# Kernel tuning notes

Measured on AMD Instinct MI355X. Metric: run time of the kernel, lower is better.

The kernel has to match this reference:

```python
import jax, jax.numpy as jnp
import numpy as np

N_OBJ = 256   # number of RoIs/objects
C = 151       # num_obj_classes (Visual Genome)
H = 512       # hidden_dim == output_dim
T = 3         # time_step


def setup_inputs() -> dict:
    key = jax.random.key(0)
    ks = jax.random.split(key, 12)
    s = jnp.float32(0.02)

    def lin(k, out_dim, in_dim):
        k1, k2 = jax.random.split(k)
        w = jax.random.normal(k1, (out_dim, in_dim), jnp.float32) * s
        b = jax.random.normal(k2, (out_dim,), jnp.float32) * s
        return w, b

    inp = {}
    inp['input_ggnn'] = jax.random.normal(ks[0], (N_OBJ, H), jnp.float32)
    inp['matrix'] = jax.random.uniform(ks[1], (C, C), jnp.float32)
    for i, name in enumerate(['eq3_w', 'eq3_u', 'eq4_w', 'eq4_u', 'eq5_w', 'eq5_u']):
        in_dim = 2 * H if name.endswith('_w') else H
        w, b = lin(ks[2 + i], H, in_dim)
        inp['w_' + name] = w
        inp['b_' + name] = b
    w, b = lin(ks[8], H, 2 * H)
    inp['w_out'], inp['b_out'] = w, b
    w, b = lin(ks[9], C, C * H)
    inp['w_cls'], inp['b_cls'] = w, b
    return inp


def _ggnn_obj(input_ggnn, matrix,
              w_eq3_w, b_eq3_w, w_eq3_u, b_eq3_u,
              w_eq4_w, b_eq4_w, w_eq4_u, b_eq4_u,
              w_eq5_w, b_eq5_w, w_eq5_u, b_eq5_u,
              w_out, b_out, w_cls, b_cls):
    n = input_ggnn.shape[0]
    # hidden[i, c] = input_ggnn[i] for every class slot c  -> [N, C, H]
    hidden0 = jnp.broadcast_to(input_ggnn[:, None, :], (n, C, H))

    def step(hidden, _):
        hidden_sum = hidden.sum(axis=0)                # [C, H]
        x = hidden_sum[None, :, :] - hidden            # [N, C, H]
        # matrix.T @ x_i  and  matrix @ x_i, vectorized over N
        av1 = jnp.einsum('cd,nch->ndh', matrix, x)     # M^T propagation
        av2 = jnp.einsum('dc,nch->ndh', matrix, x)     # M propagation
        av = jnp.concatenate([av1, av2], axis=-1).reshape(n * C, 2 * H)
        h = hidden.reshape(n * C, H)
        zv = jax.nn.sigmoid(av @ w_eq3_w.T + b_eq3_w + h @ w_eq3_u.T + b_eq3_u)
        rv = jax.nn.sigmoid(av @ w_eq4_w.T + b_eq4_w + h @ w_eq4_u.T + b_eq4_u)
        hv = jnp.tanh(av @ w_eq5_w.T + b_eq5_w + (rv * h) @ w_eq5_u.T + b_eq5_u)
        h = (1.0 - zv) * h + zv * hv
        return h.reshape(n, C, H), None

    hidden, _ = jax.lax.scan(step, hidden0, None, length=T)

    inp_rep = hidden0.reshape(n * C, H)                # input repeated per class slot
    out = jnp.concatenate([hidden.reshape(n * C, H), inp_rep], axis=1)  # [N*C, 2H]
    out = jax.nn.relu(out @ w_out.T + b_out)           # [N*C, H]
    obj_dists = out.reshape(n, C * H) @ w_cls.T + b_cls  # [N, C]
    return obj_dists


def reference(input_ggnn, matrix,
              w_eq3_w, b_eq3_w, w_eq3_u, b_eq3_u,
              w_eq4_w, b_eq4_w, w_eq4_u, b_eq4_u,
              w_eq5_w, b_eq5_w, w_eq5_u, b_eq5_u,
              w_out, b_out, w_cls, b_cls):
    return _ggnn_obj(input_ggnn, matrix,
                     w_eq3_w, b_eq3_w, w_eq3_u, b_eq3_u,
                     w_eq4_w, b_eq4_w, w_eq4_u, b_eq4_u,
                     w_eq5_w, b_eq5_w, w_eq5_u, b_eq5_u,
                     w_out, b_out, w_cls, b_cls)
```

## Files before the change

kernel.cpp:

```cpp
#include <hip/hip_runtime.h>


#define C_     151
#define H_     512
#define NOBJ   256
#define NR     38656
#define NCH    64
#define CH     9664
#define CHP    9728
#define KPAD   160
#define KLDS   168
#define KA     2560
#define KV     3584
#define KB     2560

typedef _Float16 half8 __attribute__((ext_vector_type(8)));
typedef _Float16 half4 __attribute__((ext_vector_type(4)));
typedef float    f32x4 __attribute__((ext_vector_type(4)));

__device__ __forceinline__ float sigm(float x) { return 1.f / (1.f + expf(-x)); }

__device__ __forceinline__ void gload16(const void* g, void* l) {
    __builtin_amdgcn_global_load_lds(
        (const __attribute__((address_space(1))) void*)g,
        (__attribute__((address_space(3))) void*)l, 16, 0, 0);
}

__device__ __forceinline__ int kqswz(int s) {
    return 8 * (((s & 3) + 8 - ((s >> 2) & 3) - ((s >> 4) & 3)) & 3);
}
__device__ __forceinline__ int fraswz(int lane) {
    const int lb = lane & 15;
    return lb * 32 + 8 * (((lane >> 4) + lb + (lb >> 2)) & 3);
}

__device__ __forceinline__ half8 loadA8(const _Float16* p) { return *(const half8*)p; }
__device__ __forceinline__ half8 loadA8(const float* p) {
    f32x4 a = *(const f32x4*)p;
    f32x4 b = *(const f32x4*)(p + 4);
    half8 o;
    #pragma unroll
    for (int j = 0; j < 4; ++j) { o[j] = (_Float16)a[j]; o[4 + j] = (_Float16)b[j]; }
    return o;
}

template<int OP, typename AT, bool DUPK>
__global__ __launch_bounds__(256, 2)
void gemm_kernel(const AT* __restrict__ A, int lda,
                 const _Float16* __restrict__ B, int ldb,
                 void* __restrict__ Out, int ldo,
                 const float* __restrict__ bias,
                 const float* __restrict__ bias2,
                 int kchunk, int chunkStride)
{
    constexpr bool A16 = (sizeof(AT) == 2);
    __shared__ _Float16 sA[128 * 32];
    __shared__ _Float16 sB[128 * 32];
    const int tid  = threadIdx.x;
    const int lane = tid & 63;
    const int w    = tid >> 6;
    const int m0   = blockIdx.x * 128;
    const int n0   = blockIdx.y * 128;
    const int kbase = blockIdx.z * kchunk;

    const int s0 = tid, s1 = tid + 256;
    const AT* Ap0 = A + (size_t)(m0 + (s0 >> 2)) * lda + kqswz(s0);
    const AT* Ap1 = A + (size_t)(m0 + (s1 >> 2)) * lda + kqswz(s1);
    const _Float16* Bp0 = B + (size_t)(n0 + (s0 >> 2)) * ldb + kbase + kqswz(s0);
    const _Float16* Bp1 = B + (size_t)(n0 + (s1 >> 2)) * ldb + kbase + kqswz(s1);
    const int la0 = 8 * s0;
    const int la1 = 8 * s1;
    _Float16* lA0 = &sA[w * 512];
    _Float16* lA1 = &sA[2048 + w * 512];
    _Float16* lB0 = &sB[w * 512];
    _Float16* lB1 = &sB[2048 + w * 512];

    f32x4 acc[4][4];
    #pragma unroll
    for (int i = 0; i < 4; ++i)
        #pragma unroll
        for (int j = 0; j < 4; ++j)
            #pragma unroll
            for (int r = 0; r < 4; ++r) acc[i][j][r] = 0.f;

    const int mrow = (w >> 1) * 64;
    const int ncol = (w & 1) * 64;
    const int fra  = fraswz(lane);

    for (int k0 = 0; k0 < kchunk; k0 += 32) {
        int kA;
        if (DUPK) kA = (k0 < 2048) ? k0 : ((k0 < 3072) ? k0 - 2048 : k0 - 1024);
        else      kA = kbase + k0;
        if constexpr (A16) {
            __syncthreads();
            gload16(Ap0 + kA, lA0);
            gload16(Ap1 + kA, lA1);
            gload16(Bp0 + k0, lB0);
            gload16(Bp1 + k0, lB1);
            __syncthreads();
        } else {
            half8 va0 = loadA8(Ap0 + kA);
            half8 va1 = loadA8(Ap1 + kA);
            half8 vb0 = *(const half8*)(Bp0 + k0);
            half8 vb1 = *(const half8*)(Bp1 + k0);
            __syncthreads();
            *(half8*)&sA[la0] = va0;
            *(half8*)&sA[la1] = va1;
            *(half8*)&sB[la0] = vb0;
            *(half8*)&sB[la1] = vb1;
            __syncthreads();
        }
        half8 af[4], bf[4];
        #pragma unroll
        for (int i = 0; i < 4; ++i)
            af[i] = *(const half8*)&sA[(mrow + i * 16) * 32 + fra];
        #pragma unroll
        for (int i = 0; i < 4; ++i)
            bf[i] = *(const half8*)&sB[(ncol + i * 16) * 32 + fra];
        #pragma unroll
        for (int mi = 0; mi < 4; ++mi)
            #pragma unroll
            for (int ni = 0; ni < 4; ++ni)
                acc[mi][ni] = __builtin_amdgcn_mfma_f32_16x16x32_f16(af[mi], bf[ni], acc[mi][ni], 0, 0, 0);
    }

    const size_t zoff = (size_t)blockIdx.z * (size_t)chunkStride;
    #pragma unroll
    for (int mi = 0; mi < 4; ++mi) {
        #pragma unroll
        for (int ni = 0; ni < 4; ++ni) {
            #pragma unroll
            for (int r = 0; r < 4; ++r) {
                const int row = m0 + mrow + mi * 16 + (lane >> 4) * 4 + r;
                const int col = n0 + ncol + ni * 16 + (lane & 15);
                float v = acc[mi][ni][r];
                const size_t o = zoff + (size_t)row * ldo + col;
                if (OP == 0) {
                    ((float*)Out)[o] = v;
                } else if (OP == 1) {
                    ((_Float16*)Out)[o] = (_Float16)v;
                } else {
                    const unsigned n = (unsigned)row / 151u;
                    v += bias[col] + bias2[n * 512u + col];
                    v = v > 0.f ? v : 0.f;
                    ((_Float16*)Out)[o] = (_Float16)v;
                }
            }
        }
    }
}

__global__ __launch_bounds__(512, 2)
void gemm256(const _Float16* __restrict__ A, const _Float16* __restrict__ B,
             _Float16* __restrict__ Out)
{
    constexpr int LDA = KA;
    constexpr int LDB = KB;
    constexpr int LDO = 1536;
    constexpr int NT  = KV / 64;
    __shared__ _Float16 lds[2][32768];

    const int tid  = threadIdx.x;
    const int lane = tid & 63;
    const int w    = tid >> 6;

    const int lin  = blockIdx.y * gridDim.x + blockIdx.x;
    const int xcd  = lin & 7;
    const int sub  = lin >> 3;
    const int wgid = (xcd < 4 ? xcd * 29 : 4 * 29 + (xcd - 4) * 28) + sub;
    const int m0   = (wgid / 6) * 256;
    const int n0   = (wgid % 6) * 256;

    const int tr  = tid >> 3;
    const int swz = ((tid & 7) ^ (tr & 7)) << 3;
    const _Float16* Ap = A + (size_t)(m0 + tr) * LDA + swz;
    const _Float16* Bp = B + (size_t)(n0 + tr) * LDB + swz;
    const int ldsbase = w << 9;

    auto stA = [&](int buf, int kAb, int r0) {
        gload16(Ap + (size_t)r0 * LDA + kAb, &lds[buf][r0 * 64 + ldsbase]);
    };
    auto stB = [&](int buf, int kBb, int r0) {
        gload16(Bp + (size_t)r0 * LDB + kBb, &lds[buf][16384 + r0 * 64 + ldsbase]);
    };

    const int lb = lane & 15;
    const int lq = lane >> 4;
    auto frag = [&](const _Float16* base, int row0, int ks) -> half8 {
        const int row = row0 + lb;
        const int kg  = ks * 4 + lq;
        return *(const half8*)&base[row * 64 + ((kg ^ (row & 7)) << 3)];
    };

    const int wm = (w >> 2) * 128;
    const int wn = (w & 3) * 64;

    f32x4 acc[8][4];
    #pragma unroll
    for (int i = 0; i < 8; ++i)
        #pragma unroll
        for (int j = 0; j < 4; ++j)
            #pragma unroll
            for (int r = 0; r < 4; ++r) acc[i][j][r] = 0.f;

    half8 a[4][2], bA[2][2], bB[2][2];

#define PHASE_MFMA(AF, BF, MO, NO) do {                                         \
    __builtin_amdgcn_s_setprio(1);                                              \
    _Pragma("unroll")                                                           \
    for (int i = 0; i < 4; ++i) {                                               \
        _Pragma("unroll")                                                       \
        for (int j = 0; j < 2; ++j) {                                           \
            _Pragma("unroll")                                                   \
            for (int ks = 0; ks < 2; ++ks)                                      \
                acc[(MO) + i][(NO) + j] =                                       \
                    __builtin_amdgcn_mfma_f32_16x16x32_f16(                     \
                        AF[i][ks], BF[j][ks], acc[(MO) + i][(NO) + j], 0, 0, 0);\
        }                                                                       \
    }                                                                           \
    __builtin_amdgcn_s_setprio(0);                                              \
} while (0)

    stB(0, 0, 0);  stB(0, 0, 64);  stB(0, 0, 128); stB(0, 0, 192);
    stA(0, 0, 0);  stA(0, 0, 64);  stA(0, 0, 128); stA(0, 0, 192);

    for (int t = 0; t < NT; ++t) {
        const _Float16* sA = &lds[t & 1][0];
        const _Float16* sB = &lds[t & 1][16384];

        asm volatile("s_waitcnt vmcnt(0)" ::: "memory");
        __builtin_amdgcn_s_barrier();
        __builtin_amdgcn_sched_barrier(0);

        if (t + 1 < NT) {
            const int kk  = (t + 1) * 64;
            const int kAb = (kk < 2048) ? kk : ((kk < 3072) ? kk - 2048 : kk - 1024);
            const int kBb = (kk < 1024) ? kk : kk - 1024;
            const int nb  = (t + 1) & 1;
            stB(nb, kBb, 0); stB(nb, kBb, 64); stB(nb, kBb, 128); stB(nb, kBb, 192);
            stA(nb, kAb, 0); stA(nb, kAb, 64); stA(nb, kAb, 128); stA(nb, kAb, 192);
        }

        #pragma unroll
        for (int i = 0; i < 4; ++i) {
            a[i][0] = frag(sA, wm + i * 16, 0);
            a[i][1] = frag(sA, wm + i * 16, 1);
        }
        #pragma unroll
        for (int j = 0; j < 2; ++j) {
            bA[j][0] = frag(sB, wn + j * 16, 0);
            bA[j][1] = frag(sB, wn + j * 16, 1);
            bB[j][0] = frag(sB, wn + 32 + j * 16, 0);
            bB[j][1] = frag(sB, wn + 32 + j * 16, 1);
        }
        PHASE_MFMA(a, bA, 0, 0);
        PHASE_MFMA(a, bB, 0, 2);

        #pragma unroll
        for (int i = 0; i < 4; ++i) {
            a[i][0] = frag(sA, wm + 64 + i * 16, 0);
            a[i][1] = frag(sA, wm + 64 + i * 16, 1);
        }
        PHASE_MFMA(a, bA, 4, 0);
        PHASE_MFMA(a, bB, 4, 2);
    }
#undef PHASE_MFMA

    #pragma unroll
    for (int mi = 0; mi < 8; ++mi) {
        #pragma unroll
        for (int ni = 0; ni < 4; ++ni) {
            #pragma unroll
            for (int r = 0; r < 4; ++r) {
                const int row = m0 + wm + mi * 16 + (lane >> 4) * 4 + r;
                const int col = n0 + wn + ni * 16 + (lane & 15);
                Out[(size_t)row * LDO + col] = (_Float16)acc[mi][ni][r];
            }
        }
    }
}

__global__ __launch_bounds__(256, 2)
void mix_kernel(const float* __restrict__ hid, const float* __restrict__ S,
                const _Float16* __restrict__ MTh, const _Float16* __restrict__ MTl,
                const _Float16* __restrict__ Mrh, const _Float16* __restrict__ Mrl,
                _Float16* __restrict__ AVH, int cbase)
{
    __shared__ _Float16 sxh[64 * KLDS];
    __shared__ _Float16 sxl[64 * KLDS];
    const int n  = blockIdx.x;
    const int h0 = blockIdx.y * 64;
    const int tid = threadIdx.x;

    #pragma unroll
    for (int i = 0; i < 5; ++i) {
        const int s  = tid + 256 * i;
        const int c  = s >> 3;
        const int hg = s & 7;
        half8 oh, ol;
        if (c < C_) {
            const float* hp = &hid[(size_t)(cbase + n * C_ + c) * H_ + h0 + hg * 8];
            const float* sp = &S[c * H_ + h0 + hg * 8];
            half8 hh;
            #pragma unroll
            for (int j = 0; j < 8; ++j) {
                const float hv = hp[j];
                const float x = sp[j] - hv;
                const _Float16 hi = (_Float16)x;
                oh[j] = hi;
                ol[j] = (_Float16)(x - (float)hi);
                hh[j] = (_Float16)hv;
            }
            *(half8*)&AVH[(size_t)(n * C_ + c) * KA + 2048 + h0 + hg * 8] = hh;
        } else {
            #pragma unroll
            for (int j = 0; j < 8; ++j) { oh[j] = (_Float16)0.f; ol[j] = (_Float16)0.f; }
        }
        #pragma unroll
        for (int j = 0; j < 8; ++j) {
            sxh[(hg * 8 + j) * KLDS + c] = oh[j];
            sxl[(hg * 8 + j) * KLDS + c] = ol[j];
        }
    }
    __syncthreads();

    const int lane = tid & 63;
    const int w    = tid >> 6;
    const _Float16* Mhi = (w >> 1) ? Mrh : MTh;
    const _Float16* Mlo = (w >> 1) ? Mrl : MTl;
    const int hb = (w & 1) * 32;

    f32x4 acc[10][2];
    #pragma unroll
    for (int i = 0; i < 10; ++i)
        #pragma unroll
        for (int j = 0; j < 2; ++j)
            #pragma unroll
            for (int r = 0; r < 4; ++r) acc[i][j][r] = 0.f;

    #pragma unroll
    for (int pass = 0; pass < 3; ++pass) {
        const _Float16* Ma = (pass == 2) ? Mlo : Mhi;
        const _Float16* X  = (pass == 1) ? sxl : sxh;
        #pragma unroll
        for (int kk = 0; kk < 5; ++kk) {
            const int k0 = kk * 32;
            half8 bf[2];
            #pragma unroll
            for (int ht = 0; ht < 2; ++ht)
                bf[ht] = *(const half8*)&X[(hb + ht * 16 + (lane & 15)) * KLDS + k0 + 8 * (lane >> 4)];
            #pragma unroll
            for (int dt = 0; dt < 10; ++dt) {
                half8 af = *(const half8*)&Ma[(dt * 16 + (lane & 15)) * KPAD + k0 + 8 * (lane >> 4)];
                acc[dt][0] = __builtin_amdgcn_mfma_f32_16x16x32_f16(af, bf[0], acc[dt][0], 0, 0, 0);
                acc[dt][1] = __builtin_amdgcn_mfma_f32_16x16x32_f16(af, bf[1], acc[dt][1], 0, 0, 0);
            }
        }
    }

    const int mixoff = (w >> 1) * 512;
    #pragma unroll
    for (int dt = 0; dt < 10; ++dt) {
        #pragma unroll
        for (int ht = 0; ht < 2; ++ht) {
            #pragma unroll
            for (int r = 0; r < 4; ++r) {
                const int d = dt * 16 + (lane >> 4) * 4 + r;
                if (d < C_) {
                    const int h = h0 + hb + ht * 16 + (lane & 15);
                    const float v = acc[dt][ht][r];
                    const _Float16 hi = (_Float16)v;
                    const _Float16 lo = (_Float16)(v - (float)hi);
                    _Float16* rowp = AVH + (size_t)(n * C_ + d) * KA + mixoff + h;
                    rowp[0]    = hi;
                    rowp[1024] = lo;
                }
            }
        }
    }
}


__global__ void k_sreduce(const float* __restrict__ hid, float* __restrict__ Stmp)
{
    const int c  = blockIdx.x;
    const int g  = blockIdx.y;
    const int hw = threadIdx.x;
    const float* p = hid + (size_t)c * H_ + hw * 8;
    float s[8];
    #pragma unroll
    for (int j = 0; j < 8; ++j) s[j] = 0.f;
    const size_t stride = (size_t)C_ * H_;
    for (int n = g * 32; n < g * 32 + 32; ++n) {
        f32x4 a = *(const f32x4*)(p + (size_t)n * stride);
        f32x4 b = *(const f32x4*)(p + (size_t)n * stride + 4);
        #pragma unroll
        for (int j = 0; j < 4; ++j) { s[j] += a[j]; s[4 + j] += b[j]; }
    }
    float* o = Stmp + (size_t)g * (C_ * H_) + c * H_ + hw * 8;
    *(f32x4*)o       = f32x4{s[0], s[1], s[2], s[3]};
    *(f32x4*)(o + 4) = f32x4{s[4], s[5], s[6], s[7]};
}

__global__ void k_sfold(const float* __restrict__ Stmp, float* __restrict__ S)
{
    const int idx = blockIdx.x * 256 + threadIdx.x;
    float s = 0.f;
    #pragma unroll
    for (int g = 0; g < 8; ++g) s += Stmp[(size_t)g * (C_ * H_) + idx];
    S[idx] = s;
}

__global__ void k_ew1(_Float16* __restrict__ pre, const float* __restrict__ hid,
                      const float* __restrict__ bz, const float* __restrict__ br, int cbase)
{
    const int idx = blockIdx.x * 256 + threadIdx.x;
    const unsigned r = idx >> 7;
    const int o4 = (idx & 127) << 2;
    const size_t base = (size_t)r * 1536;
    half4 zp = *(const half4*)&pre[base + o4];
    half4 rp = *(const half4*)&pre[base + 512 + o4];
    f32x4 hd = *(const f32x4*)&hid[(size_t)(cbase + r) * H_ + o4];
    f32x4 bz4 = *(const f32x4*)&bz[o4];
    f32x4 br4 = *(const f32x4*)&br[o4];
    half4 zs, rh;
    #pragma unroll
    for (int j = 0; j < 4; ++j) {
        float z = sigm((float)zp[j] + bz4[j]);
        float rr = sigm((float)rp[j] + br4[j]);
        zs[j] = (_Float16)z;
        rh[j] = (_Float16)(rr * hd[j]);
    }
    *(half4*)&pre[base + o4] = zs;
    *(half4*)&pre[base + 512 + o4] = rh;
}

__global__ void k_ew2(const _Float16* __restrict__ pre, const _Float16* __restrict__ p5a,
                      const _Float16* __restrict__ p5b,
                      float* __restrict__ hid, const float* __restrict__ b5, int cbase)
{
    const int idx = blockIdx.x * 256 + threadIdx.x;
    const unsigned r = idx >> 7;
    const int o4 = (idx & 127) << 2;
    const size_t base = (size_t)r * 1536;
    half4 w5 = *(const half4*)&pre[base + 1024 + o4];
    half4 pa = *(const half4*)&p5a[(size_t)r * H_ + o4];
    half4 pb = *(const half4*)&p5b[(size_t)r * H_ + o4];
    half4 zz = *(const half4*)&pre[base + o4];
    f32x4 hd = *(const f32x4*)&hid[(size_t)(cbase + r) * H_ + o4];
    f32x4 b54 = *(const f32x4*)&b5[o4];
    #pragma unroll
    for (int j = 0; j < 4; ++j) {
        float t = tanhf((float)w5[j] + (float)pa[j] + (float)pb[j] + b54[j]);
        float z = (float)zz[j];
        hd[j] = (1.f - z) * hd[j] + z * t;
    }
    *(f32x4*)&hid[(size_t)(cbase + r) * H_ + o4] = hd;
}


__global__ void prep_wbig(const float* w3w, const float* w3u,
                          const float* w4w, const float* w4u,
                          const float* w5w, const float* w5u,
                          _Float16* __restrict__ Wbig)
{
    const int idx = blockIdx.x * 256 + threadIdx.x;
    const int op = idx / KB;
    const int j = idx - op * KB;
    const int g = op >> 9, o = op & 511;
    const float* ww = (g == 0) ? w3w : (g == 1) ? w4w : w5w;
    const float* wu = (g == 0) ? w3u : (g == 1) ? w4u : w5u;
    _Float16 out;
    if (j < 1024) {
        out = (_Float16)ww[o * 1024 + j];
    } else if (j < 2048) {
        const float v = ww[o * 1024 + (j - 1024)];
        const _Float16 hi = (_Float16)v;
        out = (_Float16)(v - (float)hi);
    } else {
        out = (g < 2) ? (_Float16)wu[o * 512 + (j - 2048)] : (_Float16)0.f;
    }
    Wbig[idx] = out;
}

__global__ void prep_m(const float* __restrict__ matrix,
                       _Float16* __restrict__ MTh, _Float16* __restrict__ MTl,
                       _Float16* __restrict__ Mrh, _Float16* __restrict__ Mrl)
{
    const int idx = blockIdx.x * 256 + threadIdx.x;
    const int d = idx / KPAD, c = idx - d * KPAD;
    float vT = 0.f, vR = 0.f;
    if (d < C_ && c < C_) { vT = matrix[c * C_ + d]; vR = matrix[d * C_ + c]; }
    const _Float16 th = (_Float16)vT;
    const _Float16 rh = (_Float16)vR;
    MTh[idx] = th; MTl[idx] = (_Float16)(vT - (float)th);
    Mrh[idx] = rh; Mrl[idx] = (_Float16)(vR - (float)rh);
}

__global__ void prep_wout(const float* __restrict__ wout,
                          _Float16* __restrict__ WL, _Float16* __restrict__ WR)
{
    const int idx = blockIdx.x * 256 + threadIdx.x;
    const int o = idx >> 9, j = idx & 511;
    WL[idx] = (_Float16)wout[o * 1024 + j];
    WR[idx] = (_Float16)wout[o * 1024 + 512 + j];
}

__global__ void prep_wcls(const float* __restrict__ wcls, _Float16* __restrict__ w16)
{
    const int k = blockIdx.x * 256 + threadIdx.x;
    const int d = blockIdx.y;
    w16[(size_t)d * (C_ * H_) + k] = (_Float16)wcls[(size_t)d * (C_ * H_) + k];
}

__global__ void k_cast(const float* __restrict__ src, _Float16* __restrict__ dst, int n)
{
    const int i = blockIdx.x * 256 + threadIdx.x;
    if (i < n) dst[i] = (_Float16)src[i];
}

__global__ void prep_bias(const float* b3w, const float* b3u, const float* b4w,
                          const float* b4u, const float* b5w, const float* b5u,
                          float* bz, float* br, float* b5)
{
    const int i = threadIdx.x;
    bz[i] = b3w[i] + b3u[i];
    br[i] = b4w[i] + b4u[i];
    b5[i] = b5w[i] + b5u[i];
}

__global__ void prep_hid(const float* __restrict__ input, float* __restrict__ hid)
{
    const int idx = blockIdx.x * 256 + threadIdx.x;
    const unsigned row = idx >> 7;
    const int h4 = (idx & 127) << 2;
    const unsigned n = row / 151u;
    f32x4 v = *(const f32x4*)&input[(size_t)n * H_ + h4];
    *(f32x4*)&hid[(size_t)row * H_ + h4] = v;
}

__global__ void k_reduce(const float* __restrict__ partial, const float* __restrict__ bcls,
                         float* __restrict__ out)
{
    const int idx = blockIdx.x * 256 + threadIdx.x;
    const unsigned n = (unsigned)idx / 151u;
    const unsigned d = (unsigned)idx - n * 151u;
    float s = 0.f;
    for (int z = 0; z < C_; ++z)
        s += partial[(size_t)z * (NOBJ * 256) + n * 256 + d];
    out[idx] = s + bcls[d];
}


extern "C" void kernel_launch(void* const* d_in, const int* in_sizes, int n_in,
                              void* d_out, int out_size, void* d_ws, size_t ws_size,
                              hipStream_t stream)
{
    const float* input  = (const float*)d_in[0];
    const float* matrix = (const float*)d_in[1];
    const float* w3w = (const float*)d_in[2];
    const float* b3w = (const float*)d_in[3];
    const float* w3u = (const float*)d_in[4];
    const float* b3u = (const float*)d_in[5];
    const float* w4w = (const float*)d_in[6];
    const float* b4w = (const float*)d_in[7];
    const float* w4u = (const float*)d_in[8];
    const float* b4u = (const float*)d_in[9];
    const float* w5w = (const float*)d_in[10];
    const float* b5w = (const float*)d_in[11];
    const float* w5u = (const float*)d_in[12];
    const float* b5u = (const float*)d_in[13];
    const float* wout = (const float*)d_in[14];
    const float* bout = (const float*)d_in[15];
    const float* wcls = (const float*)d_in[16];
    const float* bcls = (const float*)d_in[17];
    float* obj = (float*)d_out;

    char* ws = (char*)d_ws;
    size_t off = 0;
    auto take = [&](size_t bytes) -> char* {
        off = (off + 255) & ~(size_t)255;
        char* p = ws + off;
        off += bytes;
        return p;
    };

    _Float16* Wbig  = (_Float16*)take((size_t)1536 * KB * 2);
    _Float16* MTh   = (_Float16*)take((size_t)KPAD * KPAD * 2);
    _Float16* MTl   = (_Float16*)take((size_t)KPAD * KPAD * 2);
    _Float16* Mrh   = (_Float16*)take((size_t)KPAD * KPAD * 2);
    _Float16* Mrl   = (_Float16*)take((size_t)KPAD * KPAD * 2);
    _Float16* W5u16 = (_Float16*)take((size_t)512 * 512 * 2);
    _Float16* WL16  = (_Float16*)take((size_t)512 * 512 * 2);
    _Float16* WR16  = (_Float16*)take((size_t)512 * 512 * 2);
    _Float16* in16  = (_Float16*)take((size_t)256 * 512 * 2);
    float*    bz    = (float*)take(512 * 4);
    float*    br    = (float*)take(512 * 4);
    float*    b5    = (float*)take(512 * 4);
    float*    Stmp  = (float*)take((size_t)8 * C_ * H_ * 4);
    float*    S32   = (float*)take((size_t)C_ * H_ * 4);
    float*    base  = (float*)take((size_t)256 * 512 * 4);
    float*    hid32 = (float*)take((size_t)NR * H_ * 4);
    _Float16* AVH   = (_Float16*)take((size_t)CHP * KA * 2);
    _Float16* prec  = (_Float16*)take((size_t)CHP * 1536 * 2);
    _Float16* p5u = AVH;
    _Float16* OUT16 = AVH;
    _Float16* Wcls16 = (_Float16*)hid32;
    float* partial = (float*)((char*)hid32 + (size_t)NOBJ * C_ * H_ * 2);

    (void)in_sizes; (void)n_in; (void)out_size; (void)ws_size;

    prep_wbig<<<dim3((1536 * KB) / 256), 256, 0, stream>>>(w3w, w3u, w4w, w4u, w5w, w5u, Wbig);
    prep_m<<<dim3((KPAD * KPAD) / 256), 256, 0, stream>>>(matrix, MTh, MTl, Mrh, Mrl);
    k_cast<<<dim3((512 * 512) / 256), 256, 0, stream>>>(w5u, W5u16, 512 * 512);
    prep_wout<<<dim3((512 * 512) / 256), 256, 0, stream>>>(wout, WL16, WR16);
    k_cast<<<dim3((256 * 512) / 256), 256, 0, stream>>>(input, in16, 256 * 512);
    prep_bias<<<dim3(1), 512, 0, stream>>>(b3w, b3u, b4w, b4u, b5w, b5u, bz, br, b5);
    prep_hid<<<dim3((NR * 128) / 256), 256, 0, stream>>>(input, hid32);
    gemm_kernel<0, _Float16, false><<<dim3(2, 4, 1), 256, 0, stream>>>(
        in16, 512, WR16, 512, base, 512, nullptr, nullptr, 512, 0);

    for (int t = 0; t < 3; ++t) {
        k_sreduce<<<dim3(C_, 8), 64, 0, stream>>>(hid32, Stmp);
        k_sfold<<<dim3((C_ * H_) / 256), 256, 0, stream>>>(Stmp, S32);
        for (int cc = 0; cc < 4; ++cc) {
            const int cbase = cc * CH;
            mix_kernel<<<dim3(NCH, 8), 256, 0, stream>>>(
                hid32, S32, MTh, MTl, Mrh, Mrl, AVH, cbase);
            gemm256<<<dim3(CHP / 256, 1536 / 256, 1), 512, 0, stream>>>(
                AVH, Wbig, prec);
            k_ew1<<<dim3((CH * 128) / 256), 256, 0, stream>>>(prec, hid32, bz, br, cbase);
            gemm_kernel<1, _Float16, false><<<dim3(CHP / 128, 4, 2), 256, 0, stream>>>(
                prec + 512, 1536, W5u16, 512, p5u, 512, nullptr, nullptr, 256, CHP * 512);
            k_ew2<<<dim3((CH * 128) / 256), 256, 0, stream>>>(
                prec, p5u, p5u + (size_t)CHP * 512, hid32, b5, cbase);
        }
    }

    gemm_kernel<2, float, false><<<dim3(NR / 128, 512 / 128, 1), 256, 0, stream>>>(
        hid32, 512, WL16, 512, OUT16, 512, bout, base, 512, 0);

    prep_wcls<<<dim3((C_ * H_) / 256, C_), 256, 0, stream>>>(wcls, Wcls16);
    gemm_kernel<0, _Float16, false><<<dim3(NOBJ / 128, 256 / 128, C_), 256, 0, stream>>>(
        OUT16, C_ * H_, Wcls16, C_ * H_, partial, 256, nullptr, nullptr, 512, NOBJ * 256);
    k_reduce<<<dim3(NR / 256), 256, 0, stream>>>(partial, bcls, obj);
}
```

Measured before the change: 2.420 ms.

## Restructure gemm256 into 4-stage LDS pipeline with K=32 tiles and register prefetch

The gemm256 main loop changes from a double-buffered K=64 tile with a full vmcnt(0) wait each iteration to a 4-buffer ring of K=32 tiles. Global-to-LDS loads run three tiles ahead, and fragments for the next tile are read into alternate register sets while the current MFMAs run. The aim is to hide global load latency and LDS read latency behind MFMA work. In exchange there are twice as many barriers per K, more registers for the doubled fragment sets, and a redundant dummy stage load at the tail.

```diff
diff --git a/kernel.cpp b/kernel.cpp
--- a/kernel.cpp
+++ b/kernel.cpp
@@ -157,8 +157,8 @@
     constexpr int LDA = KA;
     constexpr int LDB = KB;
     constexpr int LDO = 1536;
-    constexpr int NT  = KV / 64;
-    __shared__ _Float16 lds[2][32768];
+    constexpr int NT  = KV / 32;
+    __shared__ _Float16 lds[4 * 16384];
 
     const int tid  = threadIdx.x;
     const int lane = tid & 63;
@@ -171,25 +171,25 @@
     const int m0   = (wgid / 6) * 256;
     const int n0   = (wgid % 6) * 256;
 
-    const int tr  = tid >> 3;
-    const int swz = ((tid & 7) ^ (tr & 7)) << 3;
+    const int tr  = tid >> 2;
+    const int swz = (((tid & 3) ^ (tr & 3)) << 3);
     const _Float16* Ap = A + (size_t)(m0 + tr) * LDA + swz;
     const _Float16* Bp = B + (size_t)(n0 + tr) * LDB + swz;
-    const int ldsbase = w << 9;
-
-    auto stA = [&](int buf, int kAb, int r0) {
-        gload16(Ap + (size_t)r0 * LDA + kAb, &lds[buf][r0 * 64 + ldsbase]);
-    };
-    auto stB = [&](int buf, int kBb, int r0) {
-        gload16(Bp + (size_t)r0 * LDB + kBb, &lds[buf][16384 + r0 * 64 + ldsbase]);
+    const int ldsw = w << 9;
+
+    auto stage = [&](int buf, int kAb, int kBb) {
+        _Float16* L = &lds[buf * 16384];
+        gload16(Ap + kAb,                     L + ldsw);
+        gload16(Ap + (size_t)128 * LDA + kAb, L + 4096 + ldsw);
+        gload16(Bp + kBb,                     L + 8192 + ldsw);
+        gload16(Bp + (size_t)128 * LDB + kBb, L + 12288 + ldsw);
     };
 
     const int lb = lane & 15;
     const int lq = lane >> 4;
-    auto frag = [&](const _Float16* base, int row0, int ks) -> half8 {
+    auto frag = [&](const _Float16* base, int row0) -> half8 {
         const int row = row0 + lb;
-        const int kg  = ks * 4 + lq;
-        return *(const half8*)&base[row * 64 + ((kg ^ (row & 7)) << 3)];
+        return *(const half8*)&base[row * 32 + ((lq ^ (row & 3)) << 3)];
     };
 
     const int wm = (w >> 2) * 128;
@@ -203,68 +203,64 @@
             #pragma unroll
             for (int r = 0; r < 4; ++r) acc[i][j][r] = 0.f;
 
-    half8 a[4][2], bA[2][2], bB[2][2];
-
-#define PHASE_MFMA(AF, BF, MO, NO) do {                                         \
+    half8 aE[8], bE[4], aO[8], bO[4];
+
+    auto kAmap = [](int kk) { return (kk < 2048) ? kk : ((kk < 3072) ? kk - 2048 : kk - 1024); };
+    auto kBmap = [](int kk) { return (kk < 1024) ? kk : kk - 1024; };
+
+#define READF(T1, AN, BN) do {                                                  \
+    const _Float16* bufA_ = &lds[((T1) & 3) * 16384];                           \
+    const _Float16* bufB_ = bufA_ + 8192;                                       \
+    _Pragma("unroll")                                                           \
+    for (int i = 0; i < 8; ++i) AN[i] = frag(bufA_, wm + i * 16);               \
+    _Pragma("unroll")                                                           \
+    for (int j = 0; j < 4; ++j) BN[j] = frag(bufB_, wn + j * 16);               \
+} while (0)
+
+#define MFMA32(AC, BC) do {                                                     \
     __builtin_amdgcn_s_setprio(1);                                              \
     _Pragma("unroll")                                                           \
-    for (int i = 0; i < 4; ++i) {                                               \
+    for (int i = 0; i < 8; ++i)                                                 \
         _Pragma("unroll")                                                       \
-        for (int j = 0; j < 2; ++j) {                                           \
-            _Pragma("unroll")                                                   \
-            for (int ks = 0; ks < 2; ++ks)                                      \
-                acc[(MO) + i][(NO) + j] =                                       \
-                    __builtin_amdgcn_mfma_f32_16x16x32_f16(                     \
-                        AF[i][ks], BF[j][ks], acc[(MO) + i][(NO) + j], 0, 0, 0);\
-        }                                                                       \
-    }                                                                           \
+        for (int j = 0; j < 4; ++j)                                             \
+            acc[i][j] = __builtin_amdgcn_mfma_f32_16x16x32_f16(                 \
+                AC[i], BC[j], acc[i][j], 0, 0, 0);                              \
     __builtin_amdgcn_s_setprio(0);                                              \
 } while (0)
 
-    stB(0, 0, 0);  stB(0, 0, 64);  stB(0, 0, 128); stB(0, 0, 192);
-    stA(0, 0, 0);  stA(0, 0, 64);  stA(0, 0, 128); stA(0, 0, 192);
-
-    for (int t = 0; t < NT; ++t) {
-        const _Float16* sA = &lds[t & 1][0];
-        const _Float16* sB = &lds[t & 1][16384];
-
-        asm volatile("s_waitcnt vmcnt(0)" ::: "memory");
-        __builtin_amdgcn_s_barrier();
-        __builtin_amdgcn_sched_barrier(0);
-
-        if (t + 1 < NT) {
-            const int kk  = (t + 1) * 64;
-            const int kAb = (kk < 2048) ? kk : ((kk < 3072) ? kk - 2048 : kk - 1024);
-            const int kBb = (kk < 1024) ? kk : kk - 1024;
-            const int nb  = (t + 1) & 1;
-            stB(nb, kBb, 0); stB(nb, kBb, 64); stB(nb, kBb, 128); stB(nb, kBb, 192);
-            stA(nb, kAb, 0); stA(nb, kAb, 64); stA(nb, kAb, 128); stA(nb, kAb, 192);
-        }
-
-        #pragma unroll
-        for (int i = 0; i < 4; ++i) {
-            a[i][0] = frag(sA, wm + i * 16, 0);
-            a[i][1] = frag(sA, wm + i * 16, 1);
-        }
-        #pragma unroll
-        for (int j = 0; j < 2; ++j) {
-            bA[j][0] = frag(sB, wn + j * 16, 0);
-            bA[j][1] = frag(sB, wn + j * 16, 1);
-            bB[j][0] = frag(sB, wn + 32 + j * 16, 0);
-            bB[j][1] = frag(sB, wn + 32 + j * 16, 1);
-        }
-        PHASE_MFMA(a, bA, 0, 0);
-        PHASE_MFMA(a, bB, 0, 2);
-
-        #pragma unroll
-        for (int i = 0; i < 4; ++i) {
-            a[i][0] = frag(sA, wm + 64 + i * 16, 0);
-            a[i][1] = frag(sA, wm + 64 + i * 16, 1);
-        }
-        PHASE_MFMA(a, bA, 4, 0);
-        PHASE_MFMA(a, bB, 4, 2);
-    }
-#undef PHASE_MFMA
+#define TILE_STEP(T, AC, BC, AN, BN) do {                                       \
+    asm volatile("s_waitcnt vmcnt(4)" ::: "memory");                            \
+    __builtin_amdgcn_s_barrier();                                               \
+    __builtin_amdgcn_sched_barrier(0);                                          \
+    { int kks = ((T) + 3) * 32;                                                 \
+      if (kks >= KV) kks = 0;              \
+      stage(((T) + 3) & 3, kAmap(kks), kBmap(kks)); }                           \
+    READF((T) + 1, AN, BN);                                                     \
+    asm volatile("s_waitcnt lgkmcnt(12)" ::: "memory");                         \
+    __builtin_amdgcn_sched_barrier(0);                                          \
+    MFMA32(AC, BC);                                                             \
+} while (0)
+
+    stage(0, kAmap(0),  kBmap(0));
+    stage(1, kAmap(32), kBmap(32));
+    stage(2, kAmap(64), kBmap(64));
+    asm volatile("s_waitcnt vmcnt(8)" ::: "memory");
+    __builtin_amdgcn_s_barrier();
+    __builtin_amdgcn_sched_barrier(0);
+    READF(0, aE, bE);
+
+    for (int w2 = 0; w2 < (NT - 2) / 2; ++w2) {
+        const int e = 2 * w2;
+        TILE_STEP(e,     aE, bE, aO, bO);
+        TILE_STEP(e + 1, aO, bO, aE, bE);
+    }
+    TILE_STEP(NT - 2, aE, bE, aO, bO);
+    asm volatile("s_waitcnt lgkmcnt(0)" ::: "memory");
+    __builtin_amdgcn_sched_barrier(0);
+    MFMA32(aO, bO);
+#undef TILE_STEP
+#undef MFMA32
+#undef READF
 
     #pragma unroll
     for (int mi = 0; mi < 8; ++mi) {
```

Result: slower. 2.510 ms (+3.7%).

## Fuse GRU gate elementwise ops into GEMM epilogues and drop split-K

Applied to the files above, without the earlier changes.

The sigmoid gates (z, and r times h) move into the epilogue of the large gate GEMM. The tanh candidate plus the hidden-state update move into the epilogue of the W5u GEMM, which now writes fp32 hidden directly instead of two split-K halves. This removes the two separate elementwise kernels and their extra global-memory round trips over the pre-activation and hidden buffers, cutting launches per chunk. In exchange, the W5u GEMM loses its split-K parallelism, and the epilogues do uncoalesced scalar reads of hid and pre. Padding rows can also read hidden values past the chunk boundary.

```diff
diff --git a/kernel.cpp b/kernel.cpp
--- a/kernel.cpp
+++ b/kernel.cpp
@@ -51,6 +51,7 @@
                  void* __restrict__ Out, int ldo,
                  const float* __restrict__ bias,
                  const float* __restrict__ bias2,
+                 const _Float16* __restrict__ pre,
                  int kchunk, int chunkStride)
 {
     constexpr bool A16 = (sizeof(AT) == 2);
@@ -139,11 +140,19 @@
                     ((float*)Out)[o] = v;
                 } else if (OP == 1) {
                     ((_Float16*)Out)[o] = (_Float16)v;
-                } else {
+                } else if (OP == 2) {
                     const unsigned n = (unsigned)row / 151u;
                     v += bias[col] + bias2[n * 512u + col];
                     v = v > 0.f ? v : 0.f;
                     ((_Float16*)Out)[o] = (_Float16)v;
+                } else {
+                    if (row < CH) {
+                        const float z   = (float)pre[(size_t)row * 1536 + col];
+                        const float w5v = (float)pre[(size_t)row * 1536 + 1024 + col];
+                        const float t   = tanhf(w5v + v + bias[col]);
+                        float* hp = (float*)Out + (size_t)row * ldo + col;
+                        *hp = (1.f - z) * (*hp) + z * t;
+                    }
                 }
             }
         }
@@ -152,7 +161,8 @@
 
 __global__ __launch_bounds__(512, 2)
 void gemm256(const _Float16* __restrict__ A, const _Float16* __restrict__ B,
-             _Float16* __restrict__ Out)
+             _Float16* __restrict__ Out, const float* __restrict__ hid,
+             const float* __restrict__ bz, const float* __restrict__ br)
 {
     constexpr int LDA = KA;
     constexpr int LDB = KB;
@@ -274,7 +284,15 @@
             for (int r = 0; r < 4; ++r) {
                 const int row = m0 + wm + mi * 16 + (lane >> 4) * 4 + r;
                 const int col = n0 + wn + ni * 16 + (lane & 15);
-                Out[(size_t)row * LDO + col] = (_Float16)acc[mi][ni][r];
+                float v = acc[mi][ni][r];
+                if (col < 512) {
+                    v = sigm(v + bz[col]);
+                } else if (col < 1024) {
+                    const int c = col - 512;
+                    const float hv = hid[(size_t)row * 512 + c];
+                    v = sigm(v + br[c]) * hv;
+                }
+                Out[(size_t)row * LDO + col] = (_Float16)v;
             }
         }
     }
@@ -409,53 +427,6 @@
     #pragma unroll
     for (int g = 0; g < 8; ++g) s += Stmp[(size_t)g * (C_ * H_) + idx];
     S[idx] = s;
-}
-
-__global__ void k_ew1(_Float16* __restrict__ pre, const float* __restrict__ hid,
-                      const float* __restrict__ bz, const float* __restrict__ br, int cbase)
-{
-    const int idx = blockIdx.x * 256 + threadIdx.x;
-    const unsigned r = idx >> 7;
-    const int o4 = (idx & 127) << 2;
-    const size_t base = (size_t)r * 1536;
-    half4 zp = *(const half4*)&pre[base + o4];
-    half4 rp = *(const half4*)&pre[base + 512 + o4];
-    f32x4 hd = *(const f32x4*)&hid[(size_t)(cbase + r) * H_ + o4];
-    f32x4 bz4 = *(const f32x4*)&bz[o4];
-    f32x4 br4 = *(const f32x4*)&br[o4];
-    half4 zs, rh;
-    #pragma unroll
-    for (int j = 0; j < 4; ++j) {
-        float z = sigm((float)zp[j] + bz4[j]);
-        float rr = sigm((float)rp[j] + br4[j]);
-        zs[j] = (_Float16)z;
-        rh[j] = (_Float16)(rr * hd[j]);
-    }
-    *(half4*)&pre[base + o4] = zs;
-    *(half4*)&pre[base + 512 + o4] = rh;
-}
-
-__global__ void k_ew2(const _Float16* __restrict__ pre, const _Float16* __restrict__ p5a,
-                      const _Float16* __restrict__ p5b,
-                      float* __restrict__ hid, const float* __restrict__ b5, int cbase)
-{
-    const int idx = blockIdx.x * 256 + threadIdx.x;
-    const unsigned r = idx >> 7;
-    const int o4 = (idx & 127) << 2;
-    const size_t base = (size_t)r * 1536;
-    half4 w5 = *(const half4*)&pre[base + 1024 + o4];
-    half4 pa = *(const half4*)&p5a[(size_t)r * H_ + o4];
-    half4 pb = *(const half4*)&p5b[(size_t)r * H_ + o4];
-    half4 zz = *(const half4*)&pre[base + o4];
-    f32x4 hd = *(const f32x4*)&hid[(size_t)(cbase + r) * H_ + o4];
-    f32x4 b54 = *(const f32x4*)&b5[o4];
-    #pragma unroll
-    for (int j = 0; j < 4; ++j) {
-        float t = tanhf((float)w5[j] + (float)pa[j] + (float)pb[j] + b54[j]);
-        float z = (float)zz[j];
-        hd[j] = (1.f - z) * hd[j] + z * t;
-    }
-    *(f32x4*)&hid[(size_t)(cbase + r) * H_ + o4] = hd;
 }
 
 
@@ -603,7 +574,6 @@
     float*    hid32 = (float*)take((size_t)NR * H_ * 4);
     _Float16* AVH   = (_Float16*)take((size_t)CHP * KA * 2);
     _Float16* prec  = (_Float16*)take((size_t)CHP * 1536 * 2);
-    _Float16* p5u = AVH;
     _Float16* OUT16 = AVH;
     _Float16* Wcls16 = (_Float16*)hid32;
     float* partial = (float*)((char*)hid32 + (size_t)NOBJ * C_ * H_ * 2);
@@ -618,7 +588,7 @@
     prep_bias<<<dim3(1), 512, 0, stream>>>(b3w, b3u, b4w, b4u, b5w, b5u, bz, br, b5);
     prep_hid<<<dim3((NR * 128) / 256), 256, 0, stream>>>(input, hid32);
     gemm_kernel<0, _Float16, false><<<dim3(2, 4, 1), 256, 0, stream>>>(
-        in16, 512, WR16, 512, base, 512, nullptr, nullptr, 512, 0);
+        in16, 512, WR16, 512, base, 512, nullptr, nullptr, nullptr, 512, 0);
 
     for (int t = 0; t < 3; ++t) {
         k_sreduce<<<dim3(C_, 8), 64, 0, stream>>>(hid32, Stmp);
@@ -628,20 +598,18 @@
             mix_kernel<<<dim3(NCH, 8), 256, 0, stream>>>(
                 hid32, S32, MTh, MTl, Mrh, Mrl, AVH, cbase);
             gemm256<<<dim3(CHP / 256, 1536 / 256, 1), 512, 0, stream>>>(
-                AVH, Wbig, prec);
-            k_ew1<<<dim3((CH * 128) / 256), 256, 0, stream>>>(prec, hid32, bz, br, cbase);
-            gemm_kernel<1, _Float16, false><<<dim3(CHP / 128, 4, 2), 256, 0, stream>>>(
-                prec + 512, 1536, W5u16, 512, p5u, 512, nullptr, nullptr, 256, CHP * 512);
-            k_ew2<<<dim3((CH * 128) / 256), 256, 0, stream>>>(
-                prec, p5u, p5u + (size_t)CHP * 512, hid32, b5, cbase);
+                AVH, Wbig, prec, hid32 + (size_t)cbase * 512, bz, br);
+            gemm_kernel<3, _Float16, false><<<dim3(CHP / 128, 4, 1), 256, 0, stream>>>(
+                prec + 512, 1536, W5u16, 512, hid32 + (size_t)cbase * 512, 512,
+                b5, nullptr, prec, 512, 0);
         }
     }
 
     gemm_kernel<2, float, false><<<dim3(NR / 128, 512 / 128, 1), 256, 0, stream>>>(
-        hid32, 512, WL16, 512, OUT16, 512, bout, base, 512, 0);
+        hid32, 512, WL16, 512, OUT16, 512, bout, base, nullptr, 512, 0);
 
     prep_wcls<<<dim3((C_ * H_) / 256, C_), 256, 0, stream>>>(wcls, Wcls16);
     gemm_kernel<0, _Float16, false><<<dim3(NOBJ / 128, 256 / 128, C_), 256, 0, stream>>>(
-        OUT16, C_ * H_, Wcls16, C_ * H_, partial, 256, nullptr, nullptr, 512, NOBJ * 256);
+        OUT16, C_ * H_, Wcls16, C_ * H_, partial, 256, nullptr, nullptr, nullptr, 512, NOBJ * 256);
     k_reduce<<<dim3(NR / 256), 256, 0, stream>>>(partial, bcls, obj);
 }
```

Result: slower. 3.126 ms (+29.2%).
